# Kernel tuning notes

Measured on AMD Instinct MI355X. Metric: run time of the kernel, lower is better.

Reference implementation:

```python
import jax, jax.numpy as jnp
import numpy as np
import math

D_MODEL = 256
N_HEADS = 8
NUM_NODES = 20
KSIZE = 3
EPS = 1e-5


def _ln(x, g, b):
    m = jnp.mean(x, axis=-1, keepdims=True)
    v = jnp.mean(jnp.square(x - m), axis=-1, keepdims=True)
    return (x - m) * jax.lax.rsqrt(v + EPS) * g + b


def _conv1d(x_bdn, w_oik):
    # x: [B, D, N], w: [O, I, K], SAME padding, no bias
    return jax.lax.conv_general_dilated(
        x_bdn, w_oik, window_strides=(1,), padding='SAME',
        dimension_numbers=('NCH', 'OIH', 'NCH'))


def setup_inputs() -> dict:
    key = jax.random.key(0)
    ks = jax.random.split(key, 12)
    B, N, D, H, K = 8192, NUM_NODES, D_MODEL, N_HEADS, KSIZE
    s = 1.0 / math.sqrt(D * K)
    inp = {
        'x': jax.random.normal(ks[0], (B, N, D), jnp.float32),
        'wq': jax.random.normal(ks[1], (D, D, K), jnp.float32) * s,
        'wk': jax.random.normal(ks[2], (D, D, K), jnp.float32) * s,
        'wv': jax.random.normal(ks[3], (D, D, K), jnp.float32) * s,
        'gq': jnp.ones((D,), jnp.float32), 'bq': jnp.zeros((D,), jnp.float32),
        'gk': jnp.ones((D,), jnp.float32), 'bk': jnp.zeros((D,), jnp.float32),
        'gv': jnp.ones((D,), jnp.float32), 'bv': jnp.zeros((D,), jnp.float32),
        'rel_table': jax.random.normal(ks[4], (2 * N - 1, H), jnp.float32) * 0.02,
        'gbias': jax.random.normal(ks[5], (H, N, N), jnp.float32) * 0.02,
        'alpha': jnp.float32(1.0),
        'wo': jax.random.normal(ks[6], (D, D), jnp.float32) * (1.0 / math.sqrt(D)),
        'bo': jnp.zeros((D,), jnp.float32),
    }
    return inp


def reference(x, wq, wk, wv, gq, bq, gk, bk, gv, bv, rel_table, gbias, alpha, wo, bo):
    B, N, D = x.shape
    H = N_HEADS
    dk = D // H
    xp = jnp.transpose(x, (0, 2, 1))  # [B, D, N]
    q = x + _ln(jnp.transpose(_conv1d(xp, wq), (0, 2, 1)), gq, bq)
    k = x + _ln(jnp.transpose(_conv1d(xp, wk), (0, 2, 1)), gk, bk)
    v = x + _ln(jnp.transpose(_conv1d(xp, wv), (0, 2, 1)), gv, bv)
    q = q.reshape(B, N, H, dk).transpose(0, 2, 1, 3)  # [B, H, N, dk]
    k = k.reshape(B, N, H, dk).transpose(0, 2, 1, 3)
    v = v.reshape(B, N, H, dk).transpose(0, 2, 1, 3)
    scores = jnp.einsum('bhnd,bhmd->bhnm', q, k) / math.sqrt(dk)
    # relative position bias: index table [2N-1, H] -> [1, H, N, N]
    coords = jnp.arange(N)
    rel_idx = coords[:, None] - coords[None, :] + N - 1  # [N, N]
    rel_bias = rel_table[rel_idx]  # [N, N, H]
    scores = scores + jnp.transpose(rel_bias, (2, 0, 1))[None]
    scores = scores + gbias[None] * alpha
    attn = jax.nn.softmax(scores, axis=-1)
    out = jnp.einsum('bhnm,bhmd->bhnd', attn, v)  # dropout p=0
    out = out.transpose(0, 2, 1, 3).reshape(B, N, D)
    return out @ wo.T + bo
```

## Files before the change

### kernel.cpp

```cpp
#include <hip/hip_runtime.h>
#include <hip/hip_bf16.h>
#include <stdint.h>

#define BATCH 8192
#define NNODE 20
#define MROWS 163840
#define KCONV 768
#define NCONV 768

typedef __bf16 bf16x8 __attribute__((ext_vector_type(8)));
typedef float f32x4 __attribute__((ext_vector_type(4)));
typedef unsigned short u16x4 __attribute__((ext_vector_type(4)));
typedef unsigned short u16x8 __attribute__((ext_vector_type(8)));

#define GLOBAL_AS __attribute__((address_space(1)))
#define LDS_AS __attribute__((address_space(3)))

__device__ __forceinline__ void load_lds16(const void* g, void* l) {
  __builtin_amdgcn_global_load_lds((const GLOBAL_AS uint32_t*)g,
                                   (LDS_AS uint32_t*)l, 16, 0, 0);
}

__device__ __forceinline__ float bf2f(unsigned short u) {
  union { unsigned int i; float f; } x;
  x.i = ((unsigned int)u) << 16;
  return x.f;
}

__global__ void prep_kernel(const float* __restrict__ x,
                            const float* __restrict__ wq,
                            const float* __restrict__ wk,
                            const float* __restrict__ wv,
                            const float* __restrict__ wo,
                            __hip_bfloat16* __restrict__ xb,
                            __hip_bfloat16* __restrict__ WcT,
                            __hip_bfloat16* __restrict__ wob,
                            int* __restrict__ zrow) {
  const int stride = gridDim.x * blockDim.x;
  const int gid = blockIdx.x * blockDim.x + threadIdx.x;

  if (gid < 128) zrow[gid] = 0;

  const int n8 = (MROWS * 256) / 8;
  for (int i8 = gid; i8 < n8; i8 += stride) {
    const float4* xp = ((const float4*)x) + (size_t)i8 * 2;
    float4 a = xp[0];
    float4 b = xp[1];
    __align__(16) __hip_bfloat16 h[8];
    h[0] = __float2bfloat16(a.x); h[1] = __float2bfloat16(a.y);
    h[2] = __float2bfloat16(a.z); h[3] = __float2bfloat16(a.w);
    h[4] = __float2bfloat16(b.x); h[5] = __float2bfloat16(b.y);
    h[6] = __float2bfloat16(b.z); h[7] = __float2bfloat16(b.w);
    ((int4*)xb)[i8] = *(const int4*)h;
  }

  for (int idx = gid; idx < NCONV * KCONV; idx += stride) {
    int n = idx / KCONV;
    int j = idx - n * KCONV;
    int c = n >> 8, o = n & 255;
    int t = j >> 8, i = j & 255;
    const float* w = (c == 0) ? wq : (c == 1) ? wk : wv;
    WcT[idx] = __float2bfloat16(w[(o * 256 + i) * 3 + t]);
  }

  for (int idx = gid; idx < 256 * 256; idx += stride) {
    wob[idx] = __float2bfloat16(wo[idx]);
  }
}

__global__ __launch_bounds__(256) void conv_gemm_kernel(
    const __hip_bfloat16* __restrict__ xb,
    const __hip_bfloat16* __restrict__ WcT,
    __hip_bfloat16* __restrict__ y,
    const __hip_bfloat16* __restrict__ zrow) {
  __shared__ __align__(16) __hip_bfloat16 As[128 * 64];
  __shared__ __align__(16) __hip_bfloat16 Bs[128 * 64];

  const int tid = threadIdx.x;
  const int lane = tid & 63;
  const int wave = tid >> 6;
  const int wm = (wave >> 1) << 6;
  const int wn = (wave & 1) << 6;
  const int l16 = lane & 15;
  const int quad = lane >> 4;
  const int m0 = blockIdx.x * 128;
  const int n0 = blockIdx.y * 128;

  const __hip_bfloat16* a_base[4];
  const __hip_bfloat16* z_base[4];
  const __hip_bfloat16* b_base[4];
  int a_node[4];
  int lds_off[4];
#pragma unroll
  for (int it = 0; it < 4; ++it) {
    int flat = ((it * 4 + wave) << 6) + lane;
    int row = flat >> 3;
    int seg = flat & 7;
    int seg_g = seg ^ (row & 7);
    int gr = m0 + row;
    int b = gr / 20;
    int node = gr - b * 20;
    a_node[it] = node;
    a_base[it] = xb + (long)(gr - 1) * 256 + seg_g * 8;
    z_base[it] = zrow + seg_g * 8;
    b_base[it] = WcT + (size_t)(n0 + row) * KCONV + seg_g * 8;
    lds_off[it] = (it * 4 + wave) << 9;
  }

  f32x4 acc[4][4];
  const f32x4 zero = {0.f, 0.f, 0.f, 0.f};
#pragma unroll
  for (int i = 0; i < 4; ++i)
#pragma unroll
    for (int j = 0; j < 4; ++j) acc[i][j] = zero;

  for (int kt = 0; kt < 12; ++kt) {
    const int t = kt >> 2;
    const int i0 = (kt & 3) << 6;
    const int k0 = kt << 6;
#pragma unroll
    for (int it = 0; it < 4; ++it) {
      bool ok = (unsigned)(a_node[it] + t - 1) < 20u;
      const __hip_bfloat16* ga = ok ? (a_base[it] + t * 256 + i0) : z_base[it];
      load_lds16(ga, &As[lds_off[it]]);
      load_lds16(b_base[it] + k0, &Bs[lds_off[it]]);
    }
    __syncthreads();

#pragma unroll
    for (int kk = 0; kk < 64; kk += 32) {
      const int sx = (((kk >> 3) + quad) ^ (l16 & 7)) << 3;
      bf16x8 af[4], bfr[4];
#pragma unroll
      for (int i = 0; i < 4; ++i)
        af[i] = *(const bf16x8*)&As[((wm + i * 16 + l16) << 6) + sx];
#pragma unroll
      for (int j = 0; j < 4; ++j)
        bfr[j] = *(const bf16x8*)&Bs[((wn + j * 16 + l16) << 6) + sx];
#pragma unroll
      for (int i = 0; i < 4; ++i)
#pragma unroll
        for (int j = 0; j < 4; ++j)
          acc[i][j] = __builtin_amdgcn_mfma_f32_16x16x32_bf16(af[i], bfr[j],
                                                              acc[i][j], 0, 0, 0);
    }
    __syncthreads();
  }

#pragma unroll
  for (int i = 0; i < 4; ++i)
#pragma unroll
    for (int j = 0; j < 4; ++j)
#pragma unroll
      for (int r = 0; r < 4; ++r) {
        int row = m0 + wm + i * 16 + quad * 4 + r;
        int col = n0 + wn + j * 16 + l16;
        y[(size_t)row * NCONV + col] = __float2bfloat16(acc[i][j][r]);
      }
}

#define YST 776
__global__ __launch_bounds__(256) void attn3_kernel(
    const __hip_bfloat16* __restrict__ y,
    const __hip_bfloat16* __restrict__ xb,
    const float* __restrict__ rel,
    const float* __restrict__ gbias,
    const float* __restrict__ alpha_p,
    const float* __restrict__ gq, const float* __restrict__ bq,
    const float* __restrict__ gk, const float* __restrict__ bk,
    const float* __restrict__ gv, const float* __restrict__ bv,
    __hip_bfloat16* __restrict__ ao) {
  __shared__ __align__(16) __hip_bfloat16 yS[20 * YST];
  __shared__ __align__(16) float scS[8 * 400];
  __shared__ __align__(16) __hip_bfloat16 pS[8 * 32 * 32];
  __shared__ __align__(16) __hip_bfloat16 vT[8 * 32 * 32];

  const int b = blockIdx.x;
  const int tid = threadIdx.x;
  const float alpha = alpha_p[0];
  const int lane = tid & 63;
  const int wave = tid >> 6;
  const int l16 = lane & 15;
  const int quad = lane >> 4;

  const int4* src4 = (const int4*)(y + (size_t)b * NNODE * 768);
#pragma unroll
  for (int p = 0; p < 8; ++p) {
    int idx = tid + p * 256;
    if (idx < 1920) {
      int r = idx / 96;
      int c = idx - r * 96;
      *(int4*)&yS[r * YST + c * 8] = src4[idx];
    }
  }
  {
    const int4 z4 = {0, 0, 0, 0};
#pragma unroll
    for (int p = 0; p < 4; ++p) ((int4*)pS)[tid + p * 256] = z4;
#pragma unroll
    for (int p = 0; p < 4; ++p) ((int4*)vT)[tid + p * 256] = z4;
  }
#pragma unroll
  for (int p = 0; p < 4; ++p) {
    int idx = tid + p * 256;
    if (idx < 800) {
      int h = idx / 100;
      int rem = idx - h * 100;
      int i = rem / 5;
      int j0 = (rem - i * 5) * 4;
      float4 gb = ((const float4*)gbias)[idx];
      float4 o;
      o.x = gb.x * alpha + rel[(i - j0 + 19) * 8 + h];
      o.y = gb.y * alpha + rel[(i - j0 + 18) * 8 + h];
      o.z = gb.z * alpha + rel[(i - j0 + 17) * 8 + h];
      o.w = gb.w * alpha + rel[(i - j0 + 16) * 8 + h];
      *(float4*)&scS[idx * 4] = o;
    }
  }
  u16x8 xr[8];
  if (tid < 240) {
    const int rc = tid >> 2;
    const int p = tid & 3;
    const int r = rc / 3;
    const unsigned short* xp =
        (const unsigned short*)&xb[(((size_t)b * NNODE + r) << 8) + p * 64];
#pragma unroll
    for (int s = 0; s < 8; ++s) xr[s] = *(const u16x8*)&xp[s * 8];
  }
  __syncthreads();

  if (tid < 240) {
    const int rc = tid >> 2;
    const int p = tid & 3;
    const int r = rc / 3;
    const int c = rc - r * 3;
    unsigned short* lp = (unsigned short*)&yS[r * YST + c * 256 + p * 64];

    float sum = 0.f, sq = 0.f;
#pragma unroll
    for (int s = 0; s < 8; ++s) {
      u16x8 v = *(const u16x8*)&lp[s * 8];
#pragma unroll
      for (int e = 0; e < 8; ++e) {
        float t = bf2f(v[e]);
        sum += t;
        sq += t * t;
      }
    }
    sum += __shfl_xor(sum, 1, 64); sq += __shfl_xor(sq, 1, 64);
    sum += __shfl_xor(sum, 2, 64); sq += __shfl_xor(sq, 2, 64);

    const float mean = sum * (1.0f / 256.0f);
    const float var = sq * (1.0f / 256.0f) - mean * mean;
    const float rstd = rsqrtf(var + 1e-5f);

    const float* g = (c == 0) ? gq : (c == 1) ? gk : gv;
    const float* bb = (c == 0) ? bq : (c == 1) ? bk : bv;

#pragma unroll
    for (int s = 0; s < 8; ++s) {
      u16x8 v = *(const u16x8*)&lp[s * 8];
      u16x8 xv = xr[s];
      float4 g0 = *(const float4*)&g[p * 64 + s * 8];
      float4 g1 = *(const float4*)&g[p * 64 + s * 8 + 4];
      float4 b0 = *(const float4*)&bb[p * 64 + s * 8];
      float4 b1 = *(const float4*)&bb[p * 64 + s * 8 + 4];
      const float* gf0 = (const float*)&g0;
      const float* gf1 = (const float*)&g1;
      const float* bf0 = (const float*)&b0;
      const float* bf1 = (const float*)&b1;
      __align__(16) __hip_bfloat16 h[8];
#pragma unroll
      for (int e = 0; e < 4; ++e)
        h[e] = __float2bfloat16(bf2f(xv[e]) +
                                (bf2f(v[e]) - mean) * rstd * gf0[e] + bf0[e]);
#pragma unroll
      for (int e = 0; e < 4; ++e)
        h[4 + e] = __float2bfloat16(bf2f(xv[4 + e]) +
                                    (bf2f(v[4 + e]) - mean) * rstd * gf1[e] +
                                    bf1[e]);
      *(int4*)&lp[s * 8] = *(const int4*)h;
    }
  }
  __syncthreads();

  {
    const int h = tid >> 5, dk = tid & 31;
    const unsigned short* vcol = (const unsigned short*)yS + 512 + h * 32 + dk;
    __align__(16) unsigned short tmp[20];
#pragma unroll
    for (int r = 0; r < 20; ++r) tmp[r] = vcol[r * YST];
    unsigned short* dst = (unsigned short*)&vT[(h * 32 + dk) * 32];
    *(int4*)&dst[0] = *(const int4*)&tmp[0];
    *(int4*)&dst[8] = *(const int4*)&tmp[8];
    *(int2*)&dst[16] = *(const int2*)&tmp[16];
  }
  {
    const int rA0 = l16;
    const int rA1 = (l16 + 16 < 20) ? (l16 + 16) : 19;
    const float scale = 0.17677669529663687f;
    const f32x4 zero = {0.f, 0.f, 0.f, 0.f};
#pragma unroll
    for (int hh = 0; hh < 2; ++hh) {
      const int h = wave * 2 + hh;
      bf16x8 a0 = *(const bf16x8*)&yS[rA0 * YST + h * 32 + quad * 8];
      bf16x8 a1 = *(const bf16x8*)&yS[rA1 * YST + h * 32 + quad * 8];
      bf16x8 b0 = *(const bf16x8*)&yS[rA0 * YST + 256 + h * 32 + quad * 8];
      bf16x8 b1 = *(const bf16x8*)&yS[rA1 * YST + 256 + h * 32 + quad * 8];
      f32x4 c00 = __builtin_amdgcn_mfma_f32_16x16x32_bf16(a0, b0, zero, 0, 0, 0);
      f32x4 c01 = __builtin_amdgcn_mfma_f32_16x16x32_bf16(a0, b1, zero, 0, 0, 0);
      f32x4 c10 = __builtin_amdgcn_mfma_f32_16x16x32_bf16(a1, b0, zero, 0, 0, 0);
      f32x4 c11 = __builtin_amdgcn_mfma_f32_16x16x32_bf16(a1, b1, zero, 0, 0, 0);
      float* srow = scS + h * 400;
#pragma unroll
      for (int r = 0; r < 4; ++r) {
        const int i0 = quad * 4 + r;
        srow[i0 * 20 + l16] += c00[r] * scale;
        if (l16 < 4) srow[i0 * 20 + 16 + l16] += c01[r] * scale;
        const int iB = 16 + i0;
        if (iB < 20) {
          srow[iB * 20 + l16] += c10[r] * scale;
          if (l16 < 4) srow[iB * 20 + 16 + l16] += c11[r] * scale;
        }
      }
    }
  }
  __syncthreads();

  if (tid < 160) {
    const int h = tid / 20;
    const int i = tid - h * 20;
    const float* row = scS + h * 400 + i * 20;
    float mx = row[0];
#pragma unroll
    for (int j = 1; j < 20; ++j) mx = fmaxf(mx, row[j]);
    float e[20];
    float s = 0.f;
#pragma unroll
    for (int j = 0; j < 20; ++j) {
      e[j] = __expf(row[j] - mx);
      s += e[j];
    }
    const float inv = 1.0f / s;
    __align__(16) __hip_bfloat16 hb[32];
#pragma unroll
    for (int j = 0; j < 20; ++j) hb[j] = __float2bfloat16(e[j] * inv);
#pragma unroll
    for (int j = 20; j < 32; ++j) hb[j] = __float2bfloat16(0.f);
    __hip_bfloat16* dst = &pS[(h * 32 + i) * 32];
#pragma unroll
    for (int q = 0; q < 4; ++q)
      ((int4*)dst)[q] = ((const int4*)hb)[q];
  }
  __syncthreads();

  {
    const f32x4 zero = {0.f, 0.f, 0.f, 0.f};
#pragma unroll
    for (int hh = 0; hh < 2; ++hh) {
      const int h = wave * 2 + hh;
      bf16x8 a0 = *(const bf16x8*)&pS[(h * 32 + l16) * 32 + quad * 8];
      bf16x8 a1 = *(const bf16x8*)&pS[(h * 32 + 16 + l16) * 32 + quad * 8];
      bf16x8 b0 = *(const bf16x8*)&vT[(h * 32 + l16) * 32 + quad * 8];
      bf16x8 b1 = *(const bf16x8*)&vT[(h * 32 + 16 + l16) * 32 + quad * 8];
      f32x4 c00 = __builtin_amdgcn_mfma_f32_16x16x32_bf16(a0, b0, zero, 0, 0, 0);
      f32x4 c01 = __builtin_amdgcn_mfma_f32_16x16x32_bf16(a0, b1, zero, 0, 0, 0);
      f32x4 c10 = __builtin_amdgcn_mfma_f32_16x16x32_bf16(a1, b0, zero, 0, 0, 0);
      f32x4 c11 = __builtin_amdgcn_mfma_f32_16x16x32_bf16(a1, b1, zero, 0, 0, 0);
#pragma unroll
      for (int r = 0; r < 4; ++r) {
        const int i0 = quad * 4 + r;
        ao[(((size_t)(b * 20 + i0)) << 8) + h * 32 + l16] =
            __float2bfloat16(c00[r]);
        ao[(((size_t)(b * 20 + i0)) << 8) + h * 32 + 16 + l16] =
            __float2bfloat16(c01[r]);
        const int iB = 16 + i0;
        if (iB < 20) {
          ao[(((size_t)(b * 20 + iB)) << 8) + h * 32 + l16] =
              __float2bfloat16(c10[r]);
          ao[(((size_t)(b * 20 + iB)) << 8) + h * 32 + 16 + l16] =
              __float2bfloat16(c11[r]);
        }
      }
    }
  }
}

__global__ __launch_bounds__(256) void proj_gemm_kernel(
    const __hip_bfloat16* __restrict__ ao,
    const __hip_bfloat16* __restrict__ wob,
    const float* __restrict__ bo,
    float* __restrict__ out) {
  __shared__ __align__(16) __hip_bfloat16 As[128 * 64];
  __shared__ __align__(16) __hip_bfloat16 Bs[128 * 64];

  const int tid = threadIdx.x;
  const int lane = tid & 63;
  const int wave = tid >> 6;
  const int wm = (wave >> 1) << 6;
  const int wn = (wave & 1) << 6;
  const int l16 = lane & 15;
  const int quad = lane >> 4;
  const int m0 = blockIdx.x * 128;
  const int n0 = blockIdx.y * 128;

  const __hip_bfloat16* a_base[4];
  const __hip_bfloat16* b_base[4];
  int lds_off[4];
#pragma unroll
  for (int it = 0; it < 4; ++it) {
    int flat = ((it * 4 + wave) << 6) + lane;
    int row = flat >> 3;
    int seg = flat & 7;
    int seg_g = seg ^ (row & 7);
    a_base[it] = ao + (((size_t)(m0 + row)) << 8) + seg_g * 8;
    b_base[it] = wob + (((size_t)(n0 + row)) << 8) + seg_g * 8;
    lds_off[it] = (it * 4 + wave) << 9;
  }

  f32x4 acc[4][4];
  const f32x4 zero = {0.f, 0.f, 0.f, 0.f};
#pragma unroll
  for (int i = 0; i < 4; ++i)
#pragma unroll
    for (int j = 0; j < 4; ++j) acc[i][j] = zero;

  for (int kt = 0; kt < 4; ++kt) {
    const int k0 = kt << 6;
#pragma unroll
    for (int it = 0; it < 4; ++it) {
      load_lds16(a_base[it] + k0, &As[lds_off[it]]);
      load_lds16(b_base[it] + k0, &Bs[lds_off[it]]);
    }
    __syncthreads();

#pragma unroll
    for (int kk = 0; kk < 64; kk += 32) {
      const int sx = (((kk >> 3) + quad) ^ (l16 & 7)) << 3;
      bf16x8 af[4], bfr[4];
#pragma unroll
      for (int i = 0; i < 4; ++i)
        af[i] = *(const bf16x8*)&As[((wm + i * 16 + l16) << 6) + sx];
#pragma unroll
      for (int j = 0; j < 4; ++j)
        bfr[j] = *(const bf16x8*)&Bs[((wn + j * 16 + l16) << 6) + sx];
#pragma unroll
      for (int i = 0; i < 4; ++i)
#pragma unroll
        for (int j = 0; j < 4; ++j)
          acc[i][j] = __builtin_amdgcn_mfma_f32_16x16x32_bf16(af[i], bfr[j],
                                                              acc[i][j], 0, 0, 0);
    }
    __syncthreads();
  }

#pragma unroll
  for (int i = 0; i < 4; ++i)
#pragma unroll
    for (int j = 0; j < 4; ++j) {
      int col = n0 + wn + j * 16 + l16;
      float bias = bo[col];
#pragma unroll
      for (int r = 0; r < 4; ++r) {
        int row = m0 + wm + i * 16 + quad * 4 + r;
        out[(size_t)row * 256 + col] = acc[i][j][r] + bias;
      }
    }
}

extern "C" void kernel_launch(void* const* d_in, const int* in_sizes, int n_in,
                              void* d_out, int out_size, void* d_ws, size_t ws_size,
                              hipStream_t stream) {
  const float* x     = (const float*)d_in[0];
  const float* wq    = (const float*)d_in[1];
  const float* wk    = (const float*)d_in[2];
  const float* wv    = (const float*)d_in[3];
  const float* gq    = (const float*)d_in[4];
  const float* bq    = (const float*)d_in[5];
  const float* gk    = (const float*)d_in[6];
  const float* bk    = (const float*)d_in[7];
  const float* gv    = (const float*)d_in[8];
  const float* bv    = (const float*)d_in[9];
  const float* rel   = (const float*)d_in[10];
  const float* gbias = (const float*)d_in[11];
  const float* alpha = (const float*)d_in[12];
  const float* wo    = (const float*)d_in[13];
  const float* bo    = (const float*)d_in[14];
  float* out = (float*)d_out;

  char* ws = (char*)d_ws;
  __hip_bfloat16* xb  = (__hip_bfloat16*)(ws);
  __hip_bfloat16* y   = (__hip_bfloat16*)(ws + 83886080);
  __hip_bfloat16* ao  = (__hip_bfloat16*)(ws + 335544320);
  __hip_bfloat16* WcT = (__hip_bfloat16*)(ws + 419430400);
  __hip_bfloat16* wob = (__hip_bfloat16*)(ws + 420610048);
  int*            zr  = (int*)(ws + 420741120);

  prep_kernel<<<8192, 256, 0, stream>>>(x, wq, wk, wv, wo, xb, WcT, wob, zr);
  conv_gemm_kernel<<<dim3(1280, 6), 256, 0, stream>>>(xb, WcT, y,
                                                      (const __hip_bfloat16*)zr);
  attn3_kernel<<<8192, 256, 0, stream>>>(y, xb, rel, gbias, alpha,
                                         gq, bq, gk, bk, gv, bv, ao);
  proj_gemm_kernel<<<dim3(1280, 2), 256, 0, stream>>>(ao, wob, bo, out);
}
```

Measured before the change: 861.2 us.

## Fuse output projection into attention kernel and fold bias init into MFMA accumulators

Removes the separate projection GEMM: each attention block keeps its 20x256 output in swizzled LDS and multiplies it by the output weights read directly from global memory, writing the final fp32 output. This avoids the intermediate attention-output round trip through HBM and one kernel launch. The change also folds the 1/sqrt(dk) scale into Q, seeds the score MFMAs with relative-position and graph bias instead of a separate LDS pass, reuses LDS buffers, and swaps the conv GEMM grid so blocks sharing an M tile run together. The risk is that each block re-reads the 128KB weight matrix from cache, and the projection now runs on 32-row padded tiles, wasting some MFMA work.

```diff
diff --git a/kernel.cpp b/kernel.cpp
--- a/kernel.cpp
+++ b/kernel.cpp
@@ -7,6 +7,7 @@
 #define MROWS 163840
 #define KCONV 768
 #define NCONV 768
+#define QSCALE 0.17677669529663687f
 
 typedef __bf16 bf16x8 __attribute__((ext_vector_type(8)));
 typedef float f32x4 __attribute__((ext_vector_type(4)));
@@ -83,8 +84,8 @@
   const int wn = (wave & 1) << 6;
   const int l16 = lane & 15;
   const int quad = lane >> 4;
-  const int m0 = blockIdx.x * 128;
-  const int n0 = blockIdx.y * 128;
+  const int m0 = blockIdx.y * 128;
+  const int n0 = blockIdx.x * 128;
 
   const __hip_bfloat16* a_base[4];
   const __hip_bfloat16* z_base[4];
@@ -160,7 +161,7 @@
 }
 
 #define YST 776
-__global__ __launch_bounds__(256) void attn3_kernel(
+__global__ __launch_bounds__(256) void attn4_kernel(
     const __hip_bfloat16* __restrict__ y,
     const __hip_bfloat16* __restrict__ xb,
     const float* __restrict__ rel,
@@ -169,11 +170,15 @@
     const float* __restrict__ gq, const float* __restrict__ bq,
     const float* __restrict__ gk, const float* __restrict__ bk,
     const float* __restrict__ gv, const float* __restrict__ bv,
-    __hip_bfloat16* __restrict__ ao) {
+    const __hip_bfloat16* __restrict__ wob,
+    const float* __restrict__ bo,
+    float* __restrict__ out) {
   __shared__ __align__(16) __hip_bfloat16 yS[20 * YST];
   __shared__ __align__(16) float scS[8 * 400];
-  __shared__ __align__(16) __hip_bfloat16 pS[8 * 32 * 32];
   __shared__ __align__(16) __hip_bfloat16 vT[8 * 32 * 32];
+  __hip_bfloat16* pS  = yS;
+  __hip_bfloat16* aoA = yS + 8192;
+  __hip_bfloat16* aoB = (__hip_bfloat16*)scS;
 
   const int b = blockIdx.x;
   const int tid = threadIdx.x;
@@ -182,6 +187,7 @@
   const int wave = tid >> 6;
   const int l16 = lane & 15;
   const int quad = lane >> 4;
+  const f32x4 zero = {0.f, 0.f, 0.f, 0.f};
 
   const int4* src4 = (const int4*)(y + (size_t)b * NNODE * 768);
 #pragma unroll
@@ -191,30 +197,6 @@
       int r = idx / 96;
       int c = idx - r * 96;
       *(int4*)&yS[r * YST + c * 8] = src4[idx];
-    }
-  }
-  {
-    const int4 z4 = {0, 0, 0, 0};
-#pragma unroll
-    for (int p = 0; p < 4; ++p) ((int4*)pS)[tid + p * 256] = z4;
-#pragma unroll
-    for (int p = 0; p < 4; ++p) ((int4*)vT)[tid + p * 256] = z4;
-  }
-#pragma unroll
-  for (int p = 0; p < 4; ++p) {
-    int idx = tid + p * 256;
-    if (idx < 800) {
-      int h = idx / 100;
-      int rem = idx - h * 100;
-      int i = rem / 5;
-      int j0 = (rem - i * 5) * 4;
-      float4 gb = ((const float4*)gbias)[idx];
-      float4 o;
-      o.x = gb.x * alpha + rel[(i - j0 + 19) * 8 + h];
-      o.y = gb.y * alpha + rel[(i - j0 + 18) * 8 + h];
-      o.z = gb.z * alpha + rel[(i - j0 + 17) * 8 + h];
-      o.w = gb.w * alpha + rel[(i - j0 + 16) * 8 + h];
-      *(float4*)&scS[idx * 4] = o;
     }
   }
   u16x8 xr[8];
@@ -253,6 +235,7 @@
     const float mean = sum * (1.0f / 256.0f);
     const float var = sq * (1.0f / 256.0f) - mean * mean;
     const float rstd = rsqrtf(var + 1e-5f);
+    const float osc = (c == 0) ? QSCALE : 1.0f;
 
     const float* g = (c == 0) ? gq : (c == 1) ? gk : gv;
     const float* bb = (c == 0) ? bq : (c == 1) ? bk : bv;
@@ -272,13 +255,12 @@
       __align__(16) __hip_bfloat16 h[8];
 #pragma unroll
       for (int e = 0; e < 4; ++e)
-        h[e] = __float2bfloat16(bf2f(xv[e]) +
-                                (bf2f(v[e]) - mean) * rstd * gf0[e] + bf0[e]);
+        h[e] = __float2bfloat16(
+            (bf2f(xv[e]) + (bf2f(v[e]) - mean) * rstd * gf0[e] + bf0[e]) * osc);
 #pragma unroll
       for (int e = 0; e < 4; ++e)
-        h[4 + e] = __float2bfloat16(bf2f(xv[4 + e]) +
-                                    (bf2f(v[4 + e]) - mean) * rstd * gf1[e] +
-                                    bf1[e]);
+        h[4 + e] = __float2bfloat16(
+            (bf2f(xv[4 + e]) + (bf2f(v[4 + e]) - mean) * rstd * gf1[e] + bf1[e]) * osc);
       *(int4*)&lp[s * 8] = *(const int4*)h;
     }
   }
@@ -287,19 +269,18 @@
   {
     const int h = tid >> 5, dk = tid & 31;
     const unsigned short* vcol = (const unsigned short*)yS + 512 + h * 32 + dk;
-    __align__(16) unsigned short tmp[20];
+    __align__(16) unsigned short tmp[32];
 #pragma unroll
     for (int r = 0; r < 20; ++r) tmp[r] = vcol[r * YST];
+#pragma unroll
+    for (int r = 20; r < 32; ++r) tmp[r] = 0;
     unsigned short* dst = (unsigned short*)&vT[(h * 32 + dk) * 32];
-    *(int4*)&dst[0] = *(const int4*)&tmp[0];
-    *(int4*)&dst[8] = *(const int4*)&tmp[8];
-    *(int2*)&dst[16] = *(const int2*)&tmp[16];
+#pragma unroll
+    for (int q = 0; q < 4; ++q) ((int4*)dst)[q] = ((const int4*)tmp)[q];
   }
   {
     const int rA0 = l16;
     const int rA1 = (l16 + 16 < 20) ? (l16 + 16) : 19;
-    const float scale = 0.17677669529663687f;
-    const f32x4 zero = {0.f, 0.f, 0.f, 0.f};
 #pragma unroll
     for (int hh = 0; hh < 2; ++hh) {
       const int h = wave * 2 + hh;
@@ -307,20 +288,32 @@
       bf16x8 a1 = *(const bf16x8*)&yS[rA1 * YST + h * 32 + quad * 8];
       bf16x8 b0 = *(const bf16x8*)&yS[rA0 * YST + 256 + h * 32 + quad * 8];
       bf16x8 b1 = *(const bf16x8*)&yS[rA1 * YST + 256 + h * 32 + quad * 8];
-      f32x4 c00 = __builtin_amdgcn_mfma_f32_16x16x32_bf16(a0, b0, zero, 0, 0, 0);
-      f32x4 c01 = __builtin_amdgcn_mfma_f32_16x16x32_bf16(a0, b1, zero, 0, 0, 0);
-      f32x4 c10 = __builtin_amdgcn_mfma_f32_16x16x32_bf16(a1, b0, zero, 0, 0, 0);
-      f32x4 c11 = __builtin_amdgcn_mfma_f32_16x16x32_bf16(a1, b1, zero, 0, 0, 0);
-      float* srow = scS + h * 400;
+      f32x4 c00, c01, c10, c11;
 #pragma unroll
       for (int r = 0; r < 4; ++r) {
         const int i0 = quad * 4 + r;
-        srow[i0 * 20 + l16] += c00[r] * scale;
-        if (l16 < 4) srow[i0 * 20 + 16 + l16] += c01[r] * scale;
+        const int ib = (i0 + 16 < 20) ? (i0 + 16) : 19;
+        const int j0 = l16;
+        const int jb = (l16 + 16 < 20) ? (l16 + 16) : 19;
+        c00[r] = alpha * gbias[h * 400 + i0 * 20 + j0] + rel[(i0 - j0 + 19) * 8 + h];
+        c01[r] = alpha * gbias[h * 400 + i0 * 20 + jb] + rel[(i0 - jb + 19) * 8 + h];
+        c10[r] = alpha * gbias[h * 400 + ib * 20 + j0] + rel[(ib - j0 + 19) * 8 + h];
+        c11[r] = alpha * gbias[h * 400 + ib * 20 + jb] + rel[(ib - jb + 19) * 8 + h];
+      }
+      c00 = __builtin_amdgcn_mfma_f32_16x16x32_bf16(a0, b0, c00, 0, 0, 0);
+      c01 = __builtin_amdgcn_mfma_f32_16x16x32_bf16(a0, b1, c01, 0, 0, 0);
+      c10 = __builtin_amdgcn_mfma_f32_16x16x32_bf16(a1, b0, c10, 0, 0, 0);
+      c11 = __builtin_amdgcn_mfma_f32_16x16x32_bf16(a1, b1, c11, 0, 0, 0);
+      float* srow = scS + h * 400;
+#pragma unroll
+      for (int r = 0; r < 4; ++r) {
+        const int i0 = quad * 4 + r;
+        srow[i0 * 20 + l16] = c00[r];
+        if (l16 < 4) srow[i0 * 20 + 16 + l16] = c01[r];
         const int iB = 16 + i0;
         if (iB < 20) {
-          srow[iB * 20 + l16] += c10[r] * scale;
-          if (l16 < 4) srow[iB * 20 + 16 + l16] += c11[r] * scale;
+          srow[iB * 20 + l16] = c10[r];
+          if (l16 < 4) srow[iB * 20 + 16 + l16] = c11[r];
         }
       }
     }
@@ -349,13 +342,18 @@
     for (int j = 20; j < 32; ++j) hb[j] = __float2bfloat16(0.f);
     __hip_bfloat16* dst = &pS[(h * 32 + i) * 32];
 #pragma unroll
-    for (int q = 0; q < 4; ++q)
-      ((int4*)dst)[q] = ((const int4*)hb)[q];
+    for (int q = 0; q < 4; ++q) ((int4*)dst)[q] = ((const int4*)hb)[q];
+  } else {
+    const int t = tid - 160;
+    const int h = t / 12;
+    const int jr = 20 + (t - h * 12);
+    int4* dst = (int4*)&pS[(h * 32 + jr) * 32];
+    const int4 z4 = {0, 0, 0, 0};
+    dst[0] = z4; dst[1] = z4; dst[2] = z4; dst[3] = z4;
   }
   __syncthreads();
 
   {
-    const f32x4 zero = {0.f, 0.f, 0.f, 0.f};
 #pragma unroll
     for (int hh = 0; hh < 2; ++hh) {
       const int h = wave * 2 + hh;
@@ -370,102 +368,69 @@
 #pragma unroll
       for (int r = 0; r < 4; ++r) {
         const int i0 = quad * 4 + r;
-        ao[(((size_t)(b * 20 + i0)) << 8) + h * 32 + l16] =
-            __float2bfloat16(c00[r]);
-        ao[(((size_t)(b * 20 + i0)) << 8) + h * 32 + 16 + l16] =
-            __float2bfloat16(c01[r]);
-        const int iB = 16 + i0;
-        if (iB < 20) {
-          ao[(((size_t)(b * 20 + iB)) << 8) + h * 32 + l16] =
-              __float2bfloat16(c10[r]);
-          ao[(((size_t)(b * 20 + iB)) << 8) + h * 32 + 16 + l16] =
-              __float2bfloat16(c11[r]);
+#pragma unroll
+        for (int q2 = 0; q2 < 4; ++q2) {
+          const int row = (q2 & 1) ? (16 + i0) : i0;
+          const int col = h * 32 + ((q2 & 2) ? (16 + l16) : l16);
+          const float v = (q2 == 0) ? c00[r] : (q2 == 1) ? c10[r]
+                        : (q2 == 2) ? c01[r] : c11[r];
+          const int c = col >> 3;
+          const int cs = (c & 24) | ((c & 7) ^ (row & 7));
+          __hip_bfloat16* base = (row < 16) ? aoA : aoB;
+          base[(row & 15) * 256 + (cs << 3) + (col & 7)] = __float2bfloat16(v);
         }
       }
     }
   }
-}
-
-__global__ __launch_bounds__(256) void proj_gemm_kernel(
-    const __hip_bfloat16* __restrict__ ao,
-    const __hip_bfloat16* __restrict__ wob,
-    const float* __restrict__ bo,
-    float* __restrict__ out) {
-  __shared__ __align__(16) __hip_bfloat16 As[128 * 64];
-  __shared__ __align__(16) __hip_bfloat16 Bs[128 * 64];
-
-  const int tid = threadIdx.x;
-  const int lane = tid & 63;
-  const int wave = tid >> 6;
-  const int wm = (wave >> 1) << 6;
-  const int wn = (wave & 1) << 6;
-  const int l16 = lane & 15;
-  const int quad = lane >> 4;
-  const int m0 = blockIdx.x * 128;
-  const int n0 = blockIdx.y * 128;
-
-  const __hip_bfloat16* a_base[4];
-  const __hip_bfloat16* b_base[4];
-  int lds_off[4];
-#pragma unroll
-  for (int it = 0; it < 4; ++it) {
-    int flat = ((it * 4 + wave) << 6) + lane;
-    int row = flat >> 3;
-    int seg = flat & 7;
-    int seg_g = seg ^ (row & 7);
-    a_base[it] = ao + (((size_t)(m0 + row)) << 8) + seg_g * 8;
-    b_base[it] = wob + (((size_t)(n0 + row)) << 8) + seg_g * 8;
-    lds_off[it] = (it * 4 + wave) << 9;
-  }
-
-  f32x4 acc[4][4];
-  const f32x4 zero = {0.f, 0.f, 0.f, 0.f};
-#pragma unroll
-  for (int i = 0; i < 4; ++i)
-#pragma unroll
-    for (int j = 0; j < 4; ++j) acc[i][j] = zero;
-
-  for (int kt = 0; kt < 4; ++kt) {
-    const int k0 = kt << 6;
-#pragma unroll
-    for (int it = 0; it < 4; ++it) {
-      load_lds16(a_base[it] + k0, &As[lds_off[it]]);
-      load_lds16(b_base[it] + k0, &Bs[lds_off[it]]);
-    }
-    __syncthreads();
-
-#pragma unroll
-    for (int kk = 0; kk < 64; kk += 32) {
-      const int sx = (((kk >> 3) + quad) ^ (l16 & 7)) << 3;
-      bf16x8 af[4], bfr[4];
-#pragma unroll
-      for (int i = 0; i < 4; ++i)
-        af[i] = *(const bf16x8*)&As[((wm + i * 16 + l16) << 6) + sx];
-#pragma unroll
-      for (int j = 0; j < 4; ++j)
-        bfr[j] = *(const bf16x8*)&Bs[((wn + j * 16 + l16) << 6) + sx];
-#pragma unroll
-      for (int i = 0; i < 4; ++i)
-#pragma unroll
-        for (int j = 0; j < 4; ++j)
-          acc[i][j] = __builtin_amdgcn_mfma_f32_16x16x32_bf16(af[i], bfr[j],
-                                                              acc[i][j], 0, 0, 0);
-    }
-    __syncthreads();
-  }
-
-#pragma unroll
-  for (int i = 0; i < 4; ++i)
-#pragma unroll
-    for (int j = 0; j < 4; ++j) {
-      int col = n0 + wn + j * 16 + l16;
-      float bias = bo[col];
-#pragma unroll
-      for (int r = 0; r < 4; ++r) {
-        int row = m0 + wm + i * 16 + quad * 4 + r;
-        out[(size_t)row * 256 + col] = acc[i][j][r] + bias;
-      }
-    }
+  __syncthreads();
+
+  {
+    bf16x8 af[2][8];
+#pragma unroll
+    for (int i2 = 0; i2 < 2; ++i2) {
+      const __hip_bfloat16* base = i2 ? aoB : aoA;
+#pragma unroll
+      for (int ks = 0; ks < 8; ++ks) {
+        const int c = ks * 4 + quad;
+        const int cs = (c & 24) | ((c & 7) ^ (l16 & 7));
+        af[i2][ks] = *(const bf16x8*)&base[l16 * 256 + (cs << 3)];
+      }
+    }
+    f32x4 pacc[2][4];
+#pragma unroll
+    for (int i2 = 0; i2 < 2; ++i2)
+#pragma unroll
+      for (int cc = 0; cc < 4; ++cc) pacc[i2][cc] = zero;
+
+#pragma unroll
+    for (int cc = 0; cc < 4; ++cc) {
+      const int wrow = wave * 64 + cc * 16 + l16;
+      bf16x8 wf[8];
+#pragma unroll
+      for (int ks = 0; ks < 8; ++ks)
+        wf[ks] = *(const bf16x8*)&wob[wrow * 256 + ks * 32 + quad * 8];
+#pragma unroll
+      for (int i2 = 0; i2 < 2; ++i2)
+#pragma unroll
+        for (int ks = 0; ks < 8; ++ks)
+          pacc[i2][cc] = __builtin_amdgcn_mfma_f32_16x16x32_bf16(
+              af[i2][ks], wf[ks], pacc[i2][cc], 0, 0, 0);
+    }
+
+#pragma unroll
+    for (int cc = 0; cc < 4; ++cc) {
+      const int col = wave * 64 + cc * 16 + l16;
+      const float bias = bo[col];
+#pragma unroll
+      for (int i2 = 0; i2 < 2; ++i2)
+#pragma unroll
+        for (int r = 0; r < 4; ++r) {
+          const int row = i2 * 16 + quad * 4 + r;
+          if (row < 20)
+            out[(((size_t)(b * 20 + row)) << 8) + col] = pacc[i2][cc][r] + bias;
+        }
+    }
+  }
 }
 
 extern "C" void kernel_launch(void* const* d_in, const int* in_sizes, int n_in,
@@ -491,15 +456,13 @@
   char* ws = (char*)d_ws;
   __hip_bfloat16* xb  = (__hip_bfloat16*)(ws);
   __hip_bfloat16* y   = (__hip_bfloat16*)(ws + 83886080);
-  __hip_bfloat16* ao  = (__hip_bfloat16*)(ws + 335544320);
-  __hip_bfloat16* WcT = (__hip_bfloat16*)(ws + 419430400);
-  __hip_bfloat16* wob = (__hip_bfloat16*)(ws + 420610048);
-  int*            zr  = (int*)(ws + 420741120);
+  __hip_bfloat16* WcT = (__hip_bfloat16*)(ws + 335544320);
+  __hip_bfloat16* wob = (__hip_bfloat16*)(ws + 336723968);
+  int*            zr  = (int*)(ws + 336855040);
 
   prep_kernel<<<8192, 256, 0, stream>>>(x, wq, wk, wv, wo, xb, WcT, wob, zr);
-  conv_gemm_kernel<<<dim3(1280, 6), 256, 0, stream>>>(xb, WcT, y,
+  conv_gemm_kernel<<<dim3(6, 1280), 256, 0, stream>>>(xb, WcT, y,
                                                       (const __hip_bfloat16*)zr);
-  attn3_kernel<<<8192, 256, 0, stream>>>(y, xb, rel, gbias, alpha,
-                                         gq, bq, gk, bk, gv, bv, ao);
-  proj_gemm_kernel<<<dim3(1280, 2), 256, 0, stream>>>(ao, wob, bo, out);
-}
+  attn4_kernel<<<8192, 256, 0, stream>>>(y, xb, rel, gbias, alpha,
+                                         gq, bq, gk, bk, gv, bv, wob, bo, out);
+}
```

Result: slower. 974.8 us (+13.2%).
